# Kernel tuning notes

Hardware: AMD Instinct MI355X
Metric: run time of the kernel (lower is better)

## Reference

```python
import jax, jax.numpy as jnp
import numpy as np

B, C, H, W = 2, 256, 64, 64
HEADS, SR = 8, 4
D = C // HEADS          # head dim = 32
N = H * W               # query length = 4096
EPS = 1e-5


def _conv(x, w, stride=1, pad=0, groups=1, b=None):
    out = jax.lax.conv_general_dilated(
        x, w, (stride, stride), [(pad, pad), (pad, pad)],
        dimension_numbers=('NCHW', 'OIHW', 'NCHW'),
        feature_group_count=groups)
    if b is not None:
        out = out + b[None, :, None, None]
    return out


def _bn(x, p):
    # p: [4, C] = (gamma, beta, running_mean, running_var), eval-mode BN
    g, b, m, v = p[0], p[1], p[2], p[3]
    s = g / jnp.sqrt(v + EPS)
    return (x - m[None, :, None, None]) * s[None, :, None, None] + b[None, :, None, None]


def setup_inputs() -> dict:
    key = jax.random.key(0)
    ks = iter(jax.random.split(key, 32))
    nrm = lambda shape, s=0.05: jax.random.normal(next(ks), shape, jnp.float32) * s
    def bnp():
        return jnp.stack([jnp.ones((C,), jnp.float32), jnp.zeros((C,), jnp.float32),
                          jax.random.normal(next(ks), (C,), jnp.float32) * 0.1,
                          jax.random.uniform(next(ks), (C,), jnp.float32) + 0.5])
    return dict(
        x=jax.random.normal(next(ks), (B, C, H, W), jnp.float32),
        relative_pos_enc=jax.random.normal(next(ks), (B, 2, 64, 64), jnp.float32),
        q_w=nrm((C, C, 1, 1)), q_b=jnp.zeros((C,), jnp.float32),
        kv_w=nrm((2 * C, C, 1, 1)), kv_b=jnp.zeros((2 * C,), jnp.float32),
        sr1_dw_w=nrm((C, 1, SR + 3, SR + 3)), sr1_bn1=bnp(),
        sr1_pw_w=nrm((C, 1, 1, 1), 0.5), sr1_bn2=bnp(),
        sr2_dw_w=nrm((C, 1, SR // 2 + 3, SR // 2 + 3)), sr2_bn1=bnp(),
        sr2_pw_w=nrm((C, 1, 1, 1), 0.5), sr2_bn2=bnp(),
        local_w=nrm((C, 1, 3, 3)), local_b=jnp.zeros((C,), jnp.float32),
    )


def reference(x, relative_pos_enc, q_w, q_b, kv_w, kv_b,
              sr1_dw_w, sr1_bn1, sr1_pw_w, sr1_bn2,
              sr2_dw_w, sr2_bn1, sr2_pw_w, sr2_bn2,
              local_w, local_b):
    scale = D ** -0.5
    # q: 1x1 conv -> [B, heads, N, D]; both branches use the FIRST half of heads
    q = _conv(x, q_w, b=q_b).reshape(B, HEADS, D, N).transpose(0, 1, 3, 2)
    qh = q[:, :HEADS // 2]

    def branch(dw_w, bn1, pw_w, bn2, stride, pad, rpe_slice):
        # SR path: depthwise conv + BN + ReLU, depthwise 1x1 + BN
        y = jax.nn.relu(_bn(_conv(x, dw_w, stride, pad, groups=C), bn1))
        y = _bn(_conv(y, pw_w, groups=C), bn2)
        # local 3x3 depthwise mixing with residual
        y = _conv(y, local_w, pad=1, groups=C, b=local_b) + y
        kv = _conv(y, kv_w, b=kv_b)                # [B, 2C, h', w']
        k, v = jnp.split(kv, 2, axis=1)
        L = 2 * y.shape[2] * y.shape[3]            # channel-fold doubles kv length
        k = k.reshape(B, HEADS // 2, D, L)
        v = v.reshape(B, HEADS // 2, D, L).transpose(0, 1, 3, 2)
        attn = jnp.einsum('bhnd,bhdl->bhnl', qh, k) * scale
        rpe = jax.image.resize(rpe_slice, (B, 1, N, L), method='bicubic')
        attn = jax.nn.softmax(attn + rpe, axis=-1)
        return jnp.einsum('bhnl,bhld->bhnd', attn, v)

    x1 = branch(sr1_dw_w, sr1_bn1, sr1_pw_w, sr1_bn2,
                SR, (SR + 3) // 2, relative_pos_enc[:, 0:1])
    x2 = branch(sr2_dw_w, sr2_bn1, sr2_pw_w, sr2_bn2,
                SR // 2, (SR // 2 + 3) // 2, relative_pos_enc[:, 1:2])
    out = jnp.concatenate([x1, x2], axis=-1)       # [B, heads//2, N, 2D]
    return out.reshape(B, C, H, W)
```

## Files before the change

### kernel.cpp

```cpp
#include <hip/hip_runtime.h>
#include <hip/hip_bf16.h>
#include <math.h>

#define NB 2
#define NC 256
#define HWIN 4096
#define NN 4096
#define ND 32
#define NHH 4
#define EPSV 1e-5f

typedef short short8 __attribute__((ext_vector_type(8)));
typedef float f32x4 __attribute__((ext_vector_type(4)));
typedef unsigned short u16;
typedef unsigned int u32;

#define OFF_T1   0
#define OFF_T2   262144
#define OFF_Q    1310720
#define OFF_KT1  1835008
#define OFF_VT1  1900544
#define OFF_KT2  1966080
#define OFF_VT2  2228224
#define OFF_RCT1 2490368
#define OFF_RCT2 2531328
#define OFF_WT   2695168
#define OFF_PO   2826240
#define OFF_PS   4923392
#define OFF_QWT  5054464

#define QSCALE 0.2550437314857726f
#define LOG2E  1.4426950408889634f

__device__ __forceinline__ u16 f2bf(float x) {
  unsigned u = __float_as_uint(x);
  u += 0x7fffu + ((u >> 16) & 1u);
  return (u16)(u >> 16);
}

__device__ __forceinline__ u32 pk_bf16(float a, float b) {
  __hip_bfloat162 h = __float22bfloat162_rn(make_float2(a, b));
  u32 r; __builtin_memcpy(&r, &h, 4);
  return r;
}

__device__ __forceinline__ float keysw(float t) {
  t = fabsf(t);
  float w;
  if (t < 1.f)       w = ((1.5f*t - 2.5f)*t)*t + 1.f;
  else if (t < 2.f)  w = ((-0.5f*t + 2.5f)*t - 4.f)*t + 2.f;
  else               w = 0.f;
  return w;
}

template<int KS, int STR, int PAD, int OH>
__device__ __forceinline__ void dwconv_body(int idx, const float* __restrict__ x,
    const float* __restrict__ dww, const float* __restrict__ bn1,
    const float* __restrict__ pww, const float* __restrict__ bn2,
    float* __restrict__ tout) {
  const int hw = OH*OH;
  int s = idx % hw; int c = (idx/hw) % NC; int b = idx/(hw*NC);
  int oy = s / OH, ox = s % OH;
  const float* xp = x + (b*NC + c)*HWIN;
  const float* wp = dww + c*KS*KS;
  float acc = 0.f;
  #pragma unroll
  for (int ky = 0; ky < KS; ++ky) {
    int iy = oy*STR - PAD + ky;
    if (iy < 0 || iy >= 64) continue;
    #pragma unroll
    for (int kx = 0; kx < KS; ++kx) {
      int ix = ox*STR - PAD + kx;
      if (ix < 0 || ix >= 64) continue;
      acc += xp[iy*64 + ix] * wp[ky*KS + kx];
    }
  }
  float s1 = bn1[c] * rsqrtf(bn1[3*NC + c] + EPSV);
  float z = (acc - bn1[2*NC + c])*s1 + bn1[NC + c];
  z = fmaxf(z, 0.f);
  float s2 = bn2[c] * rsqrtf(bn2[3*NC + c] + EPSV);
  z = z * (pww[c]*s2) + (bn2[NC + c] - bn2[2*NC + c]*s2);
  tout[idx] = z;
}

__device__ __forceinline__ void rpe_body(int idx, const float* __restrict__ rpe,
                                         u16* __restrict__ rcT, int L, int ch) {
  int r = idx & 63; int l = (idx >> 6) % L; int b = idx / (64*L);
  float f = ((float)l + 0.5f)*(64.f/(float)L) - 0.5f;
  int i0 = (int)floorf(f) - 1;
  const float* rp = rpe + ((b*2 + ch)*64 + r)*64;
  float v = 0.f, wsum = 0.f;
  #pragma unroll
  for (int j = 0; j < 4; ++j) {
    int i = i0 + j;
    if (i >= 0 && i < 64) {
      float w = keysw(f - (float)i);
      v += w * rp[i]; wsum += w;
    }
  }
  rcT[((size_t)(b*L + l))*80 + 4 + r] = f2bf(v / wsum);
}

__global__ void __launch_bounds__(256) prep_kernel(
    const float* __restrict__ x,
    const float* __restrict__ dw1, const float* __restrict__ bn11,
    const float* __restrict__ pw1, const float* __restrict__ bn12, float* __restrict__ t1,
    const float* __restrict__ dw2, const float* __restrict__ bn21,
    const float* __restrict__ pw2, const float* __restrict__ bn22, float* __restrict__ t2,
    const float* __restrict__ rpe, u16* __restrict__ rct1, u16* __restrict__ rct2,
    const float* __restrict__ kvw, float* __restrict__ wtp,
    const float* __restrict__ qw, float* __restrict__ qwtp) {
  int blk = blockIdx.x;
  int t = threadIdx.x;
  if (blk < 512) {
    dwconv_body<7,4,3,16>(blk*256 + t, x, dw1, bn11, pw1, bn12, t1);
  } else if (blk < 2560) {
    dwconv_body<5,2,2,32>((blk-512)*256 + t, x, dw2, bn21, pw2, bn22, t2);
  } else if (blk < 2816) {
    rpe_body((blk-2560)*256 + t, rpe, rct1, 512, 0);
  } else if (blk < 3840) {
    rpe_body((blk-2816)*256 + t, rpe, rct2, 2048, 1);
  } else if (blk < 3968) {
    int idx = (blk-3840)*256 + t;
    float4 vv = *(const float4*)(kvw + (size_t)idx*4);
    int o = idx >> 6, c4 = idx & 63;
    *(float4*)(wtp + ((size_t)(c4*512 + o))*4) = vv;
  } else {
    int idx = (blk-3968)*256 + t;
    float4 vv = *(const float4*)(qw + (size_t)idx*4);
    int oc = idx >> 6, c4 = idx & 63;
    *(float4*)(qwtp + ((size_t)(c4*128 + oc))*4) = vv;
  }
}

__global__ void __launch_bounds__(128) localkv_kernel(
    const float* __restrict__ t1in, const float* __restrict__ t2in,
    const float* __restrict__ lw, const float* __restrict__ lb,
    const float* __restrict__ wtp, const float* __restrict__ kvb,
    u16* __restrict__ kt1, u16* __restrict__ vt1,
    u16* __restrict__ kt2, u16* __restrict__ vt2,
    const float* __restrict__ x, const float* __restrict__ qwtp,
    const float* __restrict__ qb, u16* __restrict__ q) {
  __shared__ float sbuf[NC*4];
  int blk = blockIdx.x, tid = threadIdx.x;
  if (blk < 640) {
    const float* tin; u16 *kT, *vT; int OH, hw, b, s0;
    if (blk < 128) { tin = t1in; kT = kt1; vT = vt1; OH = 16; hw = 256;  b = blk >> 6;  s0 = (blk & 63)*4; }
    else { int v = blk-128; tin = t2in; kT = kt2; vT = vt2; OH = 32; hw = 1024; b = v >> 8; s0 = (v & 255)*4; }
    int oy = s0 / OH, ox0 = s0 % OH;
    int ci = tid >> 2, i = tid & 3;
    int ox = ox0 + i;
    #pragma unroll
    for (int p = 0; p < 8; ++p) {
      int c = p*32 + ci;
      const float* tp = tin + (b*NC + c)*hw;
      const float* wp = lw + c*9;
      float acc = lb[c];
      #pragma unroll
      for (int dy = 0; dy < 3; ++dy) {
        int iy = oy + dy - 1;
        if (iy < 0 || iy >= OH) continue;
        #pragma unroll
        for (int dx = 0; dx < 3; ++dx) {
          int ix = ox + dx - 1;
          if (ix < 0 || ix >= OH) continue;
          acc += tp[iy*OH + ix]*wp[dy*3 + dx];
        }
      }
      acc += tp[oy*OH + ox];
      sbuf[c*4 + i] = acc;
    }
    __syncthreads();
    float acc[4][4];
    #pragma unroll
    for (int k = 0; k < 4; ++k) {
      float bias = kvb[tid + k*128];
      #pragma unroll
      for (int j = 0; j < 4; ++j) acc[k][j] = bias;
    }
    #pragma unroll 2
    for (int c4 = 0; c4 < 64; ++c4) {
      f32x4 w0 = *(const f32x4*)(wtp + ((size_t)(c4*512 + tid))*4);
      f32x4 w1 = *(const f32x4*)(wtp + ((size_t)(c4*512 + tid + 128))*4);
      f32x4 w2 = *(const f32x4*)(wtp + ((size_t)(c4*512 + tid + 256))*4);
      f32x4 w3 = *(const f32x4*)(wtp + ((size_t)(c4*512 + tid + 384))*4);
      #pragma unroll
      for (int j = 0; j < 4; ++j) {
        f32x4 y = *(const f32x4*)(sbuf + (c4*4 + j)*4);
        #pragma unroll
        for (int jj = 0; jj < 4; ++jj) {
          acc[0][jj] += w0[j]*y[jj];
          acc[1][jj] += w1[j]*y[jj];
          acc[2][jj] += w2[j]*y[jj];
          acc[3][jj] += w3[j]*y[jj];
        }
      }
    }
    int L = 2*hw;
    #pragma unroll
    for (int k = 0; k < 4; ++k) {
      int o = tid + k*128;
      if (k < 2) {
        int hh2 = o >> 6, e = o & 1, d = (o & 63) >> 1;
        u16* kp = kT + ((size_t)((b*NHH + hh2)*L + e*hw + s0))*ND + d;
        #pragma unroll
        for (int j = 0; j < 4; ++j) kp[j*ND] = f2bf(acc[k][j]);
      } else {
        int ov = o - 256;
        int hh2 = ov >> 6, e = ov & 1, d = (ov & 63) >> 1;
        int l0v = e*hw + s0;
        u16* vp = vT + ((size_t)((b*NHH + hh2)*(L/64) + (l0v >> 6))*ND + d)*64 + (l0v & 63);
        #pragma unroll
        for (int j = 0; j < 4; ++j) vp[j] = f2bf(acc[k][j]);
      }
    }
  } else {
    int qblk = blk - 640;
    int b = qblk >> 10;
    int n0 = (qblk & 1023) * 4;
    int oc = tid;
    float bias = qb[oc];
    float acc[4];
    #pragma unroll
    for (int i = 0; i < 4; ++i) acc[i] = bias;
    const float* xb = x + (size_t)b*NC*HWIN + n0;
    #pragma unroll 2
    for (int c4 = 0; c4 < 64; ++c4) {
      f32x4 w4 = *(const f32x4*)(qwtp + ((size_t)(c4*128 + oc))*4);
      #pragma unroll
      for (int j = 0; j < 4; ++j) {
        f32x4 xv = *(const f32x4*)(xb + (size_t)(c4*4 + j)*HWIN);
        #pragma unroll
        for (int i = 0; i < 4; ++i) acc[i] += w4[j] * xv[i];
      }
    }
    int h = oc >> 5, d = oc & 31;
    u16* qp = q + (((size_t)(b*NHH + h))*NN + n0)*ND + d;
    #pragma unroll
    for (int i = 0; i < 4; ++i) qp[i*ND] = f2bf(acc[i]*QSCALE);
  }
}

__global__ void __launch_bounds__(256) attn_kernel(
    const u16* __restrict__ qbf,
    const u16* __restrict__ kt1, const u16* __restrict__ vt1, const u16* __restrict__ rct1,
    const u16* __restrict__ kt2, const u16* __restrict__ vt2, const u16* __restrict__ rct2,
    u32* __restrict__ po32, float* __restrict__ ps,
    float* __restrict__ out) {
  __shared__ u16 kbuf[64*32];
  __shared__ u16 vbuf[32*64];
  __shared__ u32 pbuf_all[4][16*32];
  int u = blockIdx.x;
  int br, b, hh, rb, chunk;
  if (u < 512) { br = 0; b = u >> 8; hh = (u >> 6) & 3; rb = u & 63; chunk = 0; }
  else { int v = u - 512; br = 1; chunk = v & 3; rb = (v >> 2) & 63; hh = (v >> 8) & 3; b = v >> 10; }
  int L = br ? 2048 : 512;
  const u16* kT  = br ? kt2 : kt1;
  const u16* vT  = br ? vt2 : vt1;
  const u16* rcT = br ? rct2 : rct1;
  int l0base = chunk * 512;
  int tid = threadIdx.x;
  int w = tid >> 6, lane = tid & 63;
  int g = lane >> 4, lo = lane & 15;
  u32* pbuf = pbuf_all[w];
  u16* pbuf16 = (u16*)pbuf;
  int n = rb*64 + w*16 + lo;

  const u16* kbase = kT + (size_t)(b*NHH + hh)*L*ND;
  const u16* vbase = vT + (size_t)(b*NHH + hh)*ND*L;
  const u16* rcTb  = rcT + (size_t)b*L*80;

  short8 qf = *(const short8*)(qbf + (((size_t)(b*NHH + hh))*NN + n)*ND + 8*g);

  float fr = ((float)n + 0.5f)*(1.f/64.f) - 0.5f;
  int ri0 = (int)floorf(fr) - 1;
  int a = (w < 2) ? rb - 2 : rb - 1;
  int rmin = a & ~3;
  float wr4[4]; float wsum = 0.f;
  #pragma unroll
  for (int j = 0; j < 4; ++j) {
    int i = ri0 + j;
    float wv = (i >= 0 && i < 64) ? keysw(fr - (float)i) : 0.f;
    wr4[j] = wv; wsum += wv;
  }
  float invw = LOG2E / wsum;
  float wt8[8];
  #pragma unroll
  for (int s = 0; s < 8; ++s) {
    float acc = 0.f;
    #pragma unroll
    for (int j = 0; j < 4; ++j)
      acc += (ri0 + j - rmin == s) ? wr4[j]*invw : 0.f;
    wt8[s] = acc;
  }
  short8 wtf;
  {
    u32 p0 = pk_bf16(wt8[0], wt8[1]), p1 = pk_bf16(wt8[2], wt8[3]);
    u32 p2 = pk_bf16(wt8[4], wt8[5]), p3 = pk_bf16(wt8[6], wt8[7]);
    uint4 uu = make_uint4(p0, p1, p2, p3);
    wtf = __builtin_bit_cast(short8, uu);
    if (g != 0) wtf = (short8)0;
  }
  const u16* rcrow0 = rcTb + (rmin + 4);

  const f32x4 zero = {0.f, 0.f, 0.f, 0.f};
  float ssum = 0.f;
  f32x4 o0 = zero, o1 = zero;

  int kr_row = tid >> 2, kr_col = (tid & 3)*8;
  int kr_sw  = ((kr_row >> 1) & 3)*8;
  int vr_row = tid >> 3, vr_col = (tid & 7)*8;
  int vr_sw  = (vr_row & 7)*8;
  int ksw = ((lo >> 1) & 3)*8;
  int vsw = (lo & 7)*8;
  int psw4 = (lo & 7)*4;
  int psw8 = (lo & 7)*8;

  auto stageLoad = [&](short8& kr, short8& vr, int l0) {
    kr = *(const short8*)(kbase + (size_t)(l0 + kr_row)*ND + kr_col);
    vr = *(const short8*)(vbase + (size_t)(l0 >> 6)*(ND*64) + vr_row*64 + vr_col);
  };
  auto stageStore = [&](short8 kr, short8 vr) {
    *(short8*)(kbuf + kr_row*32 + (kr_col ^ kr_sw)) = kr;
    *(short8*)(vbuf + vr_row*64 + (vr_col ^ vr_sw)) = vr;
  };
  auto loadRC = [&](uint4 (&rc)[4], int l0) {
    #pragma unroll
    for (int c = 0; c < 4; ++c) {
      const u16* arow = rcrow0 + (size_t)(l0 + 16*c + lo)*80;
      uint2 ra = *(const uint2*)arow;
      uint2 rb2 = *(const uint2*)(arow + 4);
      rc[c] = make_uint4(ra.x, ra.y, rb2.x, rb2.y);
    }
  };

  short8 kr, vr;
  uint4 rcA[4], rcB[4];
  stageLoad(kr, vr, l0base);
  loadRC(rcA, l0base);

  for (int t = 0; t < 8; ++t) {
    stageStore(kr, vr);
    __syncthreads();
    if (t < 7) { stageLoad(kr, vr, l0base + (t+1)*64); loadRC(rcB, l0base + (t+1)*64); }
    f32x4 s4[4];
    #pragma unroll
    for (int c = 0; c < 4; ++c) {
      short8 rcf = __builtin_bit_cast(short8, rcA[c]);
      f32x4 accr = __builtin_amdgcn_mfma_f32_16x16x32_bf16(rcf, wtf, zero, 0, 0, 0);
      short8 kf = *(const short8*)(kbuf + (16*c + lo)*32 + ((8*g) ^ ksw));
      s4[c] = __builtin_amdgcn_mfma_f32_16x16x32_bf16(kf, qf, accr, 0, 0, 0);
    }
    float psum = 0.f;
    u32 pk[8];
    #pragma unroll
    for (int c = 0; c < 4; ++c) {
      float p0 = __builtin_amdgcn_exp2f(s4[c][0]);
      float p1 = __builtin_amdgcn_exp2f(s4[c][1]);
      float p2 = __builtin_amdgcn_exp2f(s4[c][2]);
      float p3 = __builtin_amdgcn_exp2f(s4[c][3]);
      psum += (p0 + p1) + (p2 + p3);
      pk[2*c]   = pk_bf16(p0, p1);
      pk[2*c+1] = pk_bf16(p2, p3);
    }
    ssum += psum;
    #pragma unroll
    for (int c = 0; c < 4; ++c)
      *(uint2*)(pbuf + lo*32 + ((8*c + 2*g) ^ psw4)) = make_uint2(pk[2*c], pk[2*c+1]);
    short8 pf0 = *(const short8*)(pbuf16 + lo*64 + ((8*g) ^ psw8));
    short8 pf1 = *(const short8*)(pbuf16 + lo*64 + ((32 + 8*g) ^ psw8));
    short8 v00 = *(const short8*)(vbuf + lo*64 + ((8*g) ^ vsw));
    short8 v01 = *(const short8*)(vbuf + lo*64 + ((32 + 8*g) ^ vsw));
    short8 v10 = *(const short8*)(vbuf + (16 + lo)*64 + ((8*g) ^ vsw));
    short8 v11 = *(const short8*)(vbuf + (16 + lo)*64 + ((32 + 8*g) ^ vsw));
    o0 = __builtin_amdgcn_mfma_f32_16x16x32_bf16(v00, pf0, o0, 0, 0, 0);
    o1 = __builtin_amdgcn_mfma_f32_16x16x32_bf16(v10, pf0, o1, 0, 0, 0);
    o0 = __builtin_amdgcn_mfma_f32_16x16x32_bf16(v01, pf1, o0, 0, 0, 0);
    o1 = __builtin_amdgcn_mfma_f32_16x16x32_bf16(v11, pf1, o1, 0, 0, 0);
    if (t < 7) {
      #pragma unroll
      for (int j = 0; j < 4; ++j) rcA[j] = rcB[j];
    }
    __syncthreads();
  }

  ssum += __shfl_xor(ssum, 16, 64);
  ssum += __shfl_xor(ssum, 32, 64);
  if (br == 0) {
    float inv = 1.f/ssum;
    f32x4 w0 = o0*inv, w1 = o1*inv;
    float* op = out + ((size_t)((b*NC + hh*64 + rb)*64 + (w*16 + lo)))*64;
    *(f32x4*)(op + 4*g)      = w0;
    *(f32x4*)(op + 16 + 4*g) = w1;
  } else {
    int bh = b*NHH + hh;
    int row = bh*NN + n;
    u32* pop = po32 + ((size_t)chunk*32768 + row)*16;
    pop[2*g]     = pk_bf16(o0[0], o0[1]);
    pop[2*g + 1] = pk_bf16(o0[2], o0[3]);
    pop[8 + 2*g]     = pk_bf16(o1[0], o1[1]);
    pop[8 + 2*g + 1] = pk_bf16(o1[2], o1[3]);
    if (g == 0) ps[(size_t)chunk*32768 + row] = ssum;
  }
}

__global__ void __launch_bounds__(256) combine_kernel(
    const u32* __restrict__ po32, const float* __restrict__ ps,
    float* __restrict__ out) {
  int gid = blockIdx.x*256 + threadIdx.x;
  int row = gid >> 2, part = gid & 3;
  float sden = ps[row] + ps[32768 + row] + ps[65536 + row] + ps[98304 + row];
  float inv = 1.f/sden;
  float o[8];
  #pragma unroll
  for (int i = 0; i < 8; ++i) o[i] = 0.f;
  #pragma unroll
  for (int chunk = 0; chunk < 4; ++chunk) {
    const u32* pp = po32 + ((size_t)chunk*32768 + row)*16 + part*4;
    uint4 a = *(const uint4*)pp;
    u32 av[4] = {a.x, a.y, a.z, a.w};
    #pragma unroll
    for (int j = 0; j < 4; ++j) {
      o[2*j]   += __uint_as_float(av[j] << 16);
      o[2*j+1] += __uint_as_float(av[j] & 0xffff0000u);
    }
  }
  int bh = row >> 12, n = row & 4095;
  float* op = out + ((size_t)(((bh>>2)*NC + (bh&3)*64 + (n>>6))*64 + (n&63)))*64 + 32 + part*8;
  #pragma unroll
  for (int j = 0; j < 2; ++j) {
    f32x4 v = {o[4*j]*inv, o[4*j+1]*inv, o[4*j+2]*inv, o[4*j+3]*inv};
    *(f32x4*)(op + 4*j) = v;
  }
}

extern "C" void kernel_launch(void* const* d_in, const int* in_sizes, int n_in,
                              void* d_out, int out_size, void* d_ws, size_t ws_size,
                              hipStream_t stream) {
  const float* x    = (const float*)d_in[0];
  const float* rpe  = (const float*)d_in[1];
  const float* qw   = (const float*)d_in[2];
  const float* qb   = (const float*)d_in[3];
  const float* kvw  = (const float*)d_in[4];
  const float* kvb  = (const float*)d_in[5];
  const float* dw1  = (const float*)d_in[6];
  const float* bn11 = (const float*)d_in[7];
  const float* pw1  = (const float*)d_in[8];
  const float* bn12 = (const float*)d_in[9];
  const float* dw2  = (const float*)d_in[10];
  const float* bn21 = (const float*)d_in[11];
  const float* pw2  = (const float*)d_in[12];
  const float* bn22 = (const float*)d_in[13];
  const float* lw   = (const float*)d_in[14];
  const float* lb   = (const float*)d_in[15];
  float* out = (float*)d_out;
  float* ws  = (float*)d_ws;

  float* t1   = ws + OFF_T1;
  float* t2   = ws + OFF_T2;
  u16*   q    = (u16*)(ws + OFF_Q);
  u16*   kt1  = (u16*)(ws + OFF_KT1);
  u16*   vt1  = (u16*)(ws + OFF_VT1);
  u16*   kt2  = (u16*)(ws + OFF_KT2);
  u16*   vt2  = (u16*)(ws + OFF_VT2);
  u16*   rct1 = (u16*)(ws + OFF_RCT1);
  u16*   rct2 = (u16*)(ws + OFF_RCT2);
  float* wtp  = ws + OFF_WT;
  u32*   po32 = (u32*)(ws + OFF_PO);
  float* ps   = ws + OFF_PS;
  float* qwtp = ws + OFF_QWT;

  hipLaunchKernelGGL(prep_kernel, dim3(4000), dim3(256), 0, stream,
                     x, dw1, bn11, pw1, bn12, t1, dw2, bn21, pw2, bn22, t2,
                     rpe, rct1, rct2, kvw, wtp, qw, qwtp);
  hipLaunchKernelGGL(localkv_kernel, dim3(2688), dim3(128), 0, stream,
                     t1, t2, lw, lb, wtp, kvb, kt1, vt1, kt2, vt2, x, qwtp, qb, q);
  hipLaunchKernelGGL(attn_kernel, dim3(2560), dim3(256), 0, stream,
                     q, kt1, vt1, rct1, kt2, vt2, rct2, po32, ps, out);
  hipLaunchKernelGGL(combine_kernel, dim3(512), dim3(256), 0, stream,
                     po32, ps, out);
}
```

Baseline: 180.2 us.

## Retile local/kv and q projections with channel-last intermediates and larger shared tiles

The depthwise SR output is now stored channel-last, so the local 3x3 conv reads float4 over channels. The kv projection tiles 16 spatial positions per block and splits k/v across blocks. The q projection stages a 32-position x tile in shared memory and computes a 4x4 register tile per thread. The goal is fewer redundant global weight and x reads through more reuse per block, at the cost of fewer blocks (576 vs 2688), more registers and 32KB of shared memory.

After: 188.0 us. 4.3% more time.

```diff
diff --git a/kernel.cpp b/kernel.cpp
--- a/kernel.cpp
+++ b/kernel.cpp
@@ -28,6 +28,7 @@
 #define OFF_PO   2826240
 #define OFF_PS   4923392
 #define OFF_QWT  5054464
+#define OFF_LWP  5087232
 
 #define QSCALE 0.2550437314857726f
 #define LOG2E  1.4426950408889634f
@@ -80,7 +81,7 @@
   z = fmaxf(z, 0.f);
   float s2 = bn2[c] * rsqrtf(bn2[3*NC + c] + EPSV);
   z = z * (pww[c]*s2) + (bn2[NC + c] - bn2[2*NC + c]*s2);
-  tout[idx] = z;
+  tout[((size_t)(b*hw + s))*NC + c] = z;
 }
 
 __device__ __forceinline__ void rpe_body(int idx, const float* __restrict__ rpe,
@@ -109,7 +110,8 @@
     const float* __restrict__ pw2, const float* __restrict__ bn22, float* __restrict__ t2,
     const float* __restrict__ rpe, u16* __restrict__ rct1, u16* __restrict__ rct2,
     const float* __restrict__ kvw, float* __restrict__ wtp,
-    const float* __restrict__ qw, float* __restrict__ qwtp) {
+    const float* __restrict__ qw, float* __restrict__ qwp2,
+    const float* __restrict__ lw, float* __restrict__ lwp) {
   int blk = blockIdx.x;
   int t = threadIdx.x;
   if (blk < 512) {
@@ -125,37 +127,49 @@
     float4 vv = *(const float4*)(kvw + (size_t)idx*4);
     int o = idx >> 6, c4 = idx & 63;
     *(float4*)(wtp + ((size_t)(c4*512 + o))*4) = vv;
-  } else {
+  } else if (blk < 4000) {
     int idx = (blk-3968)*256 + t;
     float4 vv = *(const float4*)(qw + (size_t)idx*4);
-    int oc = idx >> 6, c4 = idx & 63;
-    *(float4*)(qwtp + ((size_t)(c4*128 + oc))*4) = vv;
-  }
-}
-
-__global__ void __launch_bounds__(128) localkv_kernel(
-    const float* __restrict__ t1in, const float* __restrict__ t2in,
-    const float* __restrict__ lw, const float* __restrict__ lb,
+    int oc = idx >> 6, c0 = (idx & 63)*4;
+    int ocq = oc >> 2, r = oc & 3;
+    qwp2[((size_t)((c0+0)*32 + ocq))*4 + r] = vv.x;
+    qwp2[((size_t)((c0+1)*32 + ocq))*4 + r] = vv.y;
+    qwp2[((size_t)((c0+2)*32 + ocq))*4 + r] = vv.z;
+    qwp2[((size_t)((c0+3)*32 + ocq))*4 + r] = vv.w;
+  } else {
+    int c = t;
+    #pragma unroll
+    for (int tp = 0; tp < 9; ++tp) lwp[tp*256 + c] = lw[c*9 + tp];
+  }
+}
+
+__global__ void __launch_bounds__(256) localkv_kernel(
+    const float* __restrict__ t1T, const float* __restrict__ t2T,
+    const float* __restrict__ lwp, const float* __restrict__ lb,
     const float* __restrict__ wtp, const float* __restrict__ kvb,
     u16* __restrict__ kt1, u16* __restrict__ vt1,
     u16* __restrict__ kt2, u16* __restrict__ vt2,
-    const float* __restrict__ x, const float* __restrict__ qwtp,
+    const float* __restrict__ x, const float* __restrict__ qwp2,
     const float* __restrict__ qb, u16* __restrict__ q) {
-  __shared__ float sbuf[NC*4];
+  __shared__ float sbuf[NC*32];
   int blk = blockIdx.x, tid = threadIdx.x;
-  if (blk < 640) {
-    const float* tin; u16 *kT, *vT; int OH, hw, b, s0;
-    if (blk < 128) { tin = t1in; kT = kt1; vT = vt1; OH = 16; hw = 256;  b = blk >> 6;  s0 = (blk & 63)*4; }
-    else { int v = blk-128; tin = t2in; kT = kt2; vT = vt2; OH = 32; hw = 1024; b = v >> 8; s0 = (v & 255)*4; }
+  if (blk < 320) {
+    int kv = blk & 1, ti = blk >> 1;
+    const float* tT; u16 *kT, *vT; int OH, hw, b, s0;
+    if (ti < 32) { tT = t1T; kT = kt1; vT = vt1; OH = 16; hw = 256;  b = ti >> 4; s0 = (ti & 15)*16; }
+    else { int v2 = ti-32; tT = t2T; kT = kt2; vT = vt2; OH = 32; hw = 1024; b = v2 >> 6; s0 = (v2 & 63)*16; }
     int oy = s0 / OH, ox0 = s0 % OH;
-    int ci = tid >> 2, i = tid & 3;
-    int ox = ox0 + i;
-    #pragma unroll
-    for (int p = 0; p < 8; ++p) {
-      int c = p*32 + ci;
-      const float* tp = tin + (b*NC + c)*hw;
-      const float* wp = lw + c*9;
-      float acc = lb[c];
+    const float* tb = tT + (size_t)b*hw*NC;
+    int cl = tid & 63, spg = tid >> 6;
+    int c0 = cl*4;
+    f32x4 wt9[9];
+    #pragma unroll
+    for (int tp = 0; tp < 9; ++tp) wt9[tp] = *(const f32x4*)(lwp + tp*256 + c0);
+    f32x4 lb4 = *(const f32x4*)(lb + c0);
+    #pragma unroll
+    for (int i = 0; i < 4; ++i) {
+      int ox = ox0 + spg*4 + i;
+      f32x4 a = lb4;
       #pragma unroll
       for (int dy = 0; dy < 3; ++dy) {
         int iy = oy + dy - 1;
@@ -164,80 +178,87 @@
         for (int dx = 0; dx < 3; ++dx) {
           int ix = ox + dx - 1;
           if (ix < 0 || ix >= OH) continue;
-          acc += tp[iy*OH + ix]*wp[dy*3 + dx];
+          f32x4 tv = *(const f32x4*)(tb + (size_t)(iy*OH + ix)*NC + c0);
+          a += tv * wt9[dy*3 + dx];
         }
       }
-      acc += tp[oy*OH + ox];
-      sbuf[c*4 + i] = acc;
+      a += *(const f32x4*)(tb + (size_t)(oy*OH + ox)*NC + c0);
+      *(f32x4*)(sbuf + (spg*4 + i)*NC + c0) = a;
     }
     __syncthreads();
-    float acc[4][4];
-    #pragma unroll
-    for (int k = 0; k < 4; ++k) {
-      float bias = kvb[tid + k*128];
-      #pragma unroll
-      for (int j = 0; j < 4; ++j) acc[k][j] = bias;
-    }
+    int ol = tid & 127, sph = tid >> 7;
+    int obase = kv*256 + ol;
+    float acc0[8], acc1[8];
+    float b0 = kvb[obase], b1 = kvb[obase + 128];
+    #pragma unroll
+    for (int j = 0; j < 8; ++j) { acc0[j] = b0; acc1[j] = b1; }
     #pragma unroll 2
     for (int c4 = 0; c4 < 64; ++c4) {
-      f32x4 w0 = *(const f32x4*)(wtp + ((size_t)(c4*512 + tid))*4);
-      f32x4 w1 = *(const f32x4*)(wtp + ((size_t)(c4*512 + tid + 128))*4);
-      f32x4 w2 = *(const f32x4*)(wtp + ((size_t)(c4*512 + tid + 256))*4);
-      f32x4 w3 = *(const f32x4*)(wtp + ((size_t)(c4*512 + tid + 384))*4);
+      f32x4 w0 = *(const f32x4*)(wtp + ((size_t)(c4*512 + obase))*4);
+      f32x4 w1 = *(const f32x4*)(wtp + ((size_t)(c4*512 + obase + 128))*4);
       #pragma unroll
-      for (int j = 0; j < 4; ++j) {
-        f32x4 y = *(const f32x4*)(sbuf + (c4*4 + j)*4);
+      for (int j2 = 0; j2 < 8; ++j2) {
+        f32x4 y4 = *(const f32x4*)(sbuf + (sph*8 + j2)*NC + c4*4);
         #pragma unroll
-        for (int jj = 0; jj < 4; ++jj) {
-          acc[0][jj] += w0[j]*y[jj];
-          acc[1][jj] += w1[j]*y[jj];
-          acc[2][jj] += w2[j]*y[jj];
-          acc[3][jj] += w3[j]*y[jj];
-        }
+        for (int j = 0; j < 4; ++j) { acc0[j2] += w0[j]*y4[j]; acc1[j2] += w1[j]*y4[j]; }
       }
     }
     int L = 2*hw;
     #pragma unroll
-    for (int k = 0; k < 4; ++k) {
-      int o = tid + k*128;
-      if (k < 2) {
-        int hh2 = o >> 6, e = o & 1, d = (o & 63) >> 1;
-        u16* kp = kT + ((size_t)((b*NHH + hh2)*L + e*hw + s0))*ND + d;
+    for (int k = 0; k < 2; ++k) {
+      const float* ap = k ? acc1 : acc0;
+      int o = obase + k*128;
+      if (kv == 0) {
+        int hh = o >> 6, e = o & 1, d = (o & 63) >> 1;
+        u16* kp = kT + ((size_t)((b*NHH + hh)*L + e*hw + s0 + sph*8))*ND + d;
         #pragma unroll
-        for (int j = 0; j < 4; ++j) kp[j*ND] = f2bf(acc[k][j]);
+        for (int j2 = 0; j2 < 8; ++j2) kp[j2*ND] = f2bf(ap[j2]);
       } else {
         int ov = o - 256;
-        int hh2 = ov >> 6, e = ov & 1, d = (ov & 63) >> 1;
-        int l0v = e*hw + s0;
-        u16* vp = vT + ((size_t)((b*NHH + hh2)*(L/64) + (l0v >> 6))*ND + d)*64 + (l0v & 63);
+        int hh = ov >> 6, e = ov & 1, d = (ov & 63) >> 1;
+        int l0v = e*hw + s0 + sph*8;
+        u16* vp = vT + ((size_t)((b*NHH + hh)*(L/64) + (l0v >> 6))*ND + d)*64 + (l0v & 63);
         #pragma unroll
-        for (int j = 0; j < 4; ++j) vp[j] = f2bf(acc[k][j]);
+        for (int j2 = 0; j2 < 8; ++j2) vp[j2] = f2bf(ap[j2]);
       }
     }
   } else {
-    int qblk = blk - 640;
-    int b = qblk >> 10;
-    int n0 = (qblk & 1023) * 4;
-    int oc = tid;
-    float bias = qb[oc];
-    float acc[4];
-    #pragma unroll
-    for (int i = 0; i < 4; ++i) acc[i] = bias;
+    int qblk = blk - 320;
+    int b = qblk >> 7;
+    int n0 = (qblk & 127) * 32;
     const float* xb = x + (size_t)b*NC*HWIN + n0;
-    #pragma unroll 2
-    for (int c4 = 0; c4 < 64; ++c4) {
-      f32x4 w4 = *(const f32x4*)(qwtp + ((size_t)(c4*128 + oc))*4);
+    #pragma unroll
+    for (int j = 0; j < 8; ++j) {
+      int u = tid + 256*j;
+      int c = u >> 3, spq = u & 7;
+      *(f32x4*)(sbuf + c*32 + spq*4) = *(const f32x4*)(xb + (size_t)c*HWIN + spq*4);
+    }
+    __syncthreads();
+    int ocq = tid & 31, spg = tid >> 5;
+    float acc[4][4];
+    #pragma unroll
+    for (int k = 0; k < 4; ++k) {
+      float bias = qb[ocq*4 + k];
       #pragma unroll
-      for (int j = 0; j < 4; ++j) {
-        f32x4 xv = *(const f32x4*)(xb + (size_t)(c4*4 + j)*HWIN);
+      for (int i = 0; i < 4; ++i) acc[k][i] = bias;
+    }
+    #pragma unroll 4
+    for (int c = 0; c < NC; ++c) {
+      f32x4 w4 = *(const f32x4*)(qwp2 + ((size_t)(c*32 + ocq))*4);
+      f32x4 y4 = *(const f32x4*)(sbuf + c*32 + spg*4);
+      #pragma unroll
+      for (int k = 0; k < 4; ++k)
         #pragma unroll
-        for (int i = 0; i < 4; ++i) acc[i] += w4[j] * xv[i];
-      }
-    }
-    int h = oc >> 5, d = oc & 31;
-    u16* qp = q + (((size_t)(b*NHH + h))*NN + n0)*ND + d;
-    #pragma unroll
-    for (int i = 0; i < 4; ++i) qp[i*ND] = f2bf(acc[i]*QSCALE);
+        for (int i = 0; i < 4; ++i) acc[k][i] += w4[k]*y4[i];
+    }
+    #pragma unroll
+    for (int k = 0; k < 4; ++k) {
+      int oc = ocq*4 + k;
+      int h = oc >> 5, d = oc & 31;
+      u16* qp = q + (((size_t)(b*NHH + h))*NN + n0 + spg*4)*ND + d;
+      #pragma unroll
+      for (int i = 0; i < 4; ++i) qp[i*ND] = f2bf(acc[k][i]*QSCALE);
+    }
   }
 }
 
@@ -468,13 +489,14 @@
   float* wtp  = ws + OFF_WT;
   u32*   po32 = (u32*)(ws + OFF_PO);
   float* ps   = ws + OFF_PS;
-  float* qwtp = ws + OFF_QWT;
-
-  hipLaunchKernelGGL(prep_kernel, dim3(4000), dim3(256), 0, stream,
+  float* qwp2 = ws + OFF_QWT;
+  float* lwp  = ws + OFF_LWP;
+
+  hipLaunchKernelGGL(prep_kernel, dim3(4001), dim3(256), 0, stream,
                      x, dw1, bn11, pw1, bn12, t1, dw2, bn21, pw2, bn22, t2,
-                     rpe, rct1, rct2, kvw, wtp, qw, qwtp);
-  hipLaunchKernelGGL(localkv_kernel, dim3(2688), dim3(128), 0, stream,
-                     t1, t2, lw, lb, wtp, kvb, kt1, vt1, kt2, vt2, x, qwtp, qb, q);
+                     rpe, rct1, rct2, kvw, wtp, qw, qwp2, lw, lwp);
+  hipLaunchKernelGGL(localkv_kernel, dim3(576), dim3(256), 0, stream,
+                     t1, t2, lwp, lb, wtp, kvb, kt1, vt1, kt2, vt2, x, qwp2, qb, q);
   hipLaunchKernelGGL(attn_kernel, dim3(2560), dim3(256), 0, stream,
                      q, kt1, vt1, rct1, kt2, vt2, rct2, po32, ps, out);
   hipLaunchKernelGGL(combine_kernel, dim3(512), dim3(256), 0, stream,
```
